# Kernel tuning notes

Hardware: AMD Instinct MI355X
Metric: run time of the kernel (lower is better)

The kernel has to match this reference:

```python
import jax, jax.numpy as jnp
import numpy as np

EMBED = 1024  # embed_dim = hidden_dim = out_dim (n_head=1)
NQ, NK = 4096, 4096
NEG = 1e16


def setup_inputs() -> dict:
    key = jax.random.key(0)
    ks = jax.random.split(key, 10)
    stdv = 1.0 / np.sqrt(EMBED)
    lin = lambda kk: jax.random.uniform(kk, (EMBED, EMBED), jnp.float32, -stdv, stdv)
    vec = lambda kk: jax.random.uniform(kk, (EMBED,), jnp.float32, -stdv, stdv)
    return {
        "q": jax.random.normal(ks[0], (NQ, EMBED), jnp.float32),
        "k": jax.random.normal(ks[1], (NK, EMBED), jnp.float32),
        "mask": jax.random.randint(ks[2], (NQ, NK), 0, 2, jnp.int32),
        "wei": jax.random.uniform(ks[3], (NQ, NK), jnp.float32),
        "Wq": lin(ks[4]), "bq": vec(ks[5]),
        "Wk": lin(ks[6]), "bk": vec(ks[7]),
        "Wp": lin(ks[8]), "bp": vec(ks[9]),
    }


def reference(q, k, mask, wei, Wq, bq, Wk, bk, Wp, bp):
    # Linear projections (torch Linear: x @ W.T + b)
    kx = k @ Wk.T + bk                      # [NK, D]
    qx = q @ Wq.T + bq                      # [NQ, D]
    # dot_product score
    score = qx @ kx.T                       # [NQ, NK]
    bias = (mask.astype(jnp.int32) - 1).astype(score.dtype) * NEG
    score = jax.nn.softmax(score + bias, axis=-1)
    # second weighted+masked softmax pass
    score = jax.nn.softmax(score * wei + bias, axis=-1)
    out = (score @ kx) @ Wp.T + bp          # [NQ, D]
    return out, score
```

## Files before the change

kernel.cpp:

```cpp
#include <hip/hip_runtime.h>


typedef __bf16 bf16;
typedef __bf16 bf16x8 __attribute__((ext_vector_type(8)));
typedef __bf16 bf16x4 __attribute__((ext_vector_type(4)));
typedef float  f32x4  __attribute__((ext_vector_type(4)));
typedef float  f32x16 __attribute__((ext_vector_type(16)));

typedef __attribute__((address_space(1))) void as1_void;
typedef __attribute__((address_space(3))) void as3_void;

#define NQ  4096
#define NKK 4096
#define EMB 1024

#define BM 128
#define BN 128
#define BK 32

__device__ __forceinline__ void gld_lds16(const void* g, void* l) {
    __builtin_amdgcn_global_load_lds((as1_void*)g, (as3_void*)l, 16, 0, 0);
}

__global__ __launch_bounds__(256) void prep_pair(
    const float* __restrict__ a, const float* __restrict__ b,
    bf16* __restrict__ ah, bf16* __restrict__ al,
    bf16* __restrict__ bh, bf16* __restrict__ bl, int n)
{
    const float* s = blockIdx.y ? b : a;
    bf16* h = blockIdx.y ? bh : ah;
    bf16* l = blockIdx.y ? bl : al;
    const int i = (blockIdx.x * 256 + threadIdx.x) * 4;
    if (i >= n) return;
    f32x4 v = *(const f32x4*)(s + i);
    bf16x4 hv, lv;
#pragma unroll
    for (int c = 0; c < 4; c++) {
        float x = v[c];
        bf16 hh = (bf16)x;
        hv[c] = hh;
        lv[c] = (bf16)(x - (float)hh);
    }
    *(bf16x4*)(h + i) = hv;
    *(bf16x4*)(l + i) = lv;
}

__global__ __launch_bounds__(256) void prep_w3(
    const float* __restrict__ w0, const float* __restrict__ w1, const float* __restrict__ w2,
    bf16* __restrict__ h0, bf16* __restrict__ l0,
    bf16* __restrict__ h1, bf16* __restrict__ l1,
    bf16* __restrict__ h2, bf16* __restrict__ l2, int n)
{
    const int z = blockIdx.y;
    const float* s = (z == 0) ? w0 : (z == 1) ? w1 : w2;
    bf16* h = (z == 0) ? h0 : (z == 1) ? h1 : h2;
    bf16* l = (z == 0) ? l0 : (z == 1) ? l1 : l2;
    const int i = (blockIdx.x * 256 + threadIdx.x) * 4;
    if (i >= n) return;
    f32x4 v = *(const f32x4*)(s + i);
    bf16x4 hv, lv;
#pragma unroll
    for (int c = 0; c < 4; c++) {
        float x = v[c];
        bf16 hh = (bf16)x;
        hv[c] = hh;
        lv[c] = (bf16)(x - (float)hh);
    }
    *(bf16x4*)(h + i) = hv;
    *(bf16x4*)(l + i) = lv;
}

__global__ __launch_bounds__(256) void transpose_bf16(
    const bf16* __restrict__ src, bf16* __restrict__ dst, int R, int C)
{
    __shared__ bf16 tile[32][33];
    const int bx = blockIdx.x * 32;
    const int by = blockIdx.y * 32;
    const int tx = threadIdx.x & 31;
    const int ty = threadIdx.x >> 5;
#pragma unroll
    for (int r = 0; r < 4; r++)
        tile[ty + 8 * r][tx] = src[(size_t)(by + ty + 8 * r) * C + bx + tx];
    __syncthreads();
#pragma unroll
    for (int r = 0; r < 4; r++)
        dst[(size_t)(bx + ty + 8 * r) * R + by + tx] = tile[tx][ty + 8 * r];
}

template<int NS, int MODE>
__global__ __launch_bounds__(256) void reduce_k(
    const float* __restrict__ P, const float* __restrict__ bias,
    float* __restrict__ of, bf16* __restrict__ oh, int n, int Nld)
{
    const int i = (blockIdx.x * 256 + threadIdx.x) * 4;
    if (i >= n) return;
    f32x4 v = *(const f32x4*)(P + i);
#pragma unroll
    for (int s = 1; s < NS; s++)
        v += *(const f32x4*)(P + (size_t)s * n + i);
    if (MODE == 1)
        v += *(const f32x4*)(bias + (i & (Nld - 1)));
    if (MODE == 0) {
        bf16x4 o;
#pragma unroll
        for (int c = 0; c < 4; c++) o[c] = (bf16)v[c];
        *(bf16x4*)(oh + i) = o;
    } else {
        *(f32x4*)(of + i) = v;
    }
}

template<int NSPLIT, int HAS_BIAS, int OUT_BF16>
__global__ __launch_bounds__(256) void gemm_bt(
    const bf16* __restrict__ A, const bf16* __restrict__ B,
    const float* __restrict__ bias,
    float* __restrict__ Cf, bf16* __restrict__ Cb,
    int M, int N, int Ksub, int lda, int ldb)
{
    __shared__ bf16 sA[BM * BK];
    __shared__ bf16 sB[BN * BK];
    const int t    = threadIdx.x;
    const int wave = t >> 6;
    const int lane = t & 63;
    const int l31  = lane & 31;
    const int lhi  = lane >> 5;
    const int wm   = wave >> 1;
    const int wn   = wave & 1;
    const int bm   = blockIdx.y * BM;
    const int bn   = blockIdx.x * BN;
    const int srow = t >> 2;
    const int gseg = (t & 3) ^ ((srow >> 1) & 3);
    const int rsw  = (l31 >> 1) & 3;
    const int kz   = (NSPLIT > 0) ? (int)blockIdx.z : 0;

    A += (size_t)kz * Ksub;
    B += (size_t)kz * Ksub;
    if (NSPLIT > 0) Cf += (size_t)kz * M * N;

    const bf16* ga = A + (size_t)(bm + srow) * lda + gseg * 8;
    const bf16* gb = B + (size_t)(bn + srow) * ldb + gseg * 8;
    char* lA = (char*)sA + wave * 1024;
    char* lB = (char*)sB + wave * 1024;

    f32x16 acc[2][2] = {};

    for (int k0 = 0; k0 < Ksub; k0 += BK) {
        __syncthreads();
        gld_lds16(ga + k0,                      lA);
        gld_lds16(ga + (size_t)64 * lda + k0,   lA + 4096);
        gld_lds16(gb + k0,                      lB);
        gld_lds16(gb + (size_t)64 * ldb + k0,   lB + 4096);
        __syncthreads();
        bf16x8 af[2][2], bfr[2][2];
#pragma unroll
        for (int mi = 0; mi < 2; mi++)
#pragma unroll
            for (int kh = 0; kh < 2; kh++)
                af[mi][kh] = *(const bf16x8*)
                    &sA[(wm * 64 + mi * 32 + l31) * BK + ((kh * 2 + lhi) ^ rsw) * 8];
#pragma unroll
        for (int nj = 0; nj < 2; nj++)
#pragma unroll
            for (int kh = 0; kh < 2; kh++)
                bfr[nj][kh] = *(const bf16x8*)
                    &sB[(wn * 64 + nj * 32 + l31) * BK + ((kh * 2 + lhi) ^ rsw) * 8];
#pragma unroll
        for (int kh = 0; kh < 2; kh++)
#pragma unroll
            for (int mi = 0; mi < 2; mi++)
#pragma unroll
                for (int nj = 0; nj < 2; nj++)
                    acc[mi][nj] = __builtin_amdgcn_mfma_f32_32x32x16_bf16(
                        af[mi][kh], bfr[nj][kh], acc[mi][nj], 0, 0, 0);
    }

#pragma unroll
    for (int mi = 0; mi < 2; mi++)
#pragma unroll
        for (int nj = 0; nj < 2; nj++) {
            const int cg = bn + wn * 64 + nj * 32 + l31;
            const float bv = HAS_BIAS ? bias[cg] : 0.0f;
#pragma unroll
            for (int r = 0; r < 16; r++) {
                const int rg = bm + wm * 64 + mi * 32 + (r & 3) + 8 * (r >> 2) + 4 * lhi;
                const float v = acc[mi][nj][r] + bv;
                const size_t idx = (size_t)rg * N + cg;
                if (NSPLIT > 0)    Cf[idx] = v;
                else if (OUT_BF16) Cb[idx] = (bf16)v;
                else               Cf[idx] = v;
            }
        }
}

template<int BATCH, int HAS_BIAS, int HILO>
__global__ __launch_bounds__(256) void gemm_bt_split(
    const bf16* __restrict__ Ah0, const bf16* __restrict__ Al0,
    const bf16* __restrict__ Bh0, const bf16* __restrict__ Bl0,
    const float* __restrict__ bias0, bf16* __restrict__ Ch0, bf16* __restrict__ Cl0,
    const bf16* __restrict__ Ah1, const bf16* __restrict__ Al1,
    const bf16* __restrict__ Bh1, const bf16* __restrict__ Bl1,
    const float* __restrict__ bias1, bf16* __restrict__ Ch1, bf16* __restrict__ Cl1,
    float* __restrict__ Cf,
    int M, int N, int K)
{
    __shared__ bf16 sAh[BM * BK], sAl[BM * BK], sBh[BN * BK], sBl[BN * BK];
    const int t    = threadIdx.x;
    const int wave = t >> 6;
    const int lane = t & 63;
    const int l31  = lane & 31;
    const int lhi  = lane >> 5;
    const int wm   = wave >> 1;
    const int wn   = wave & 1;
    const int bm   = blockIdx.y * BM;
    const int bn   = blockIdx.x * BN;
    const int srow = t >> 2;
    const int gseg = (t & 3) ^ ((srow >> 1) & 3);
    const int rsw  = (l31 >> 1) & 3;

    const int mt = BATCH ? (int)blockIdx.z : 0;

    const bf16* Ah = (BATCH && mt) ? Ah1 : Ah0;
    const bf16* Al = (BATCH && mt) ? Al1 : Al0;
    const bf16* Bh = (BATCH && mt) ? Bh1 : Bh0;
    const bf16* Bl = (BATCH && mt) ? Bl1 : Bl0;
    const float* bias = (BATCH && mt) ? bias1 : bias0;
    bf16* Ch = (BATCH && mt) ? Ch1 : Ch0;
    bf16* Cl = (BATCH && mt) ? Cl1 : Cl0;

    const size_t offA = (size_t)(bm + srow) * K + gseg * 8;
    const size_t offB = (size_t)(bn + srow) * K + gseg * 8;
    char* lAh = (char*)sAh + wave * 1024;
    char* lAl = (char*)sAl + wave * 1024;
    char* lBh = (char*)sBh + wave * 1024;
    char* lBl = (char*)sBl + wave * 1024;

    f32x16 acc[2][2] = {};

    for (int k0 = 0; k0 < K; k0 += BK) {
        __syncthreads();
        gld_lds16(Ah + offA + k0,                  lAh);
        gld_lds16(Ah + offA + (size_t)64 * K + k0, lAh + 4096);
        gld_lds16(Al + offA + k0,                  lAl);
        gld_lds16(Al + offA + (size_t)64 * K + k0, lAl + 4096);
        gld_lds16(Bh + offB + k0,                  lBh);
        gld_lds16(Bh + offB + (size_t)64 * K + k0, lBh + 4096);
        gld_lds16(Bl + offB + k0,                  lBl);
        gld_lds16(Bl + offB + (size_t)64 * K + k0, lBl + 4096);
        __syncthreads();
#pragma unroll
        for (int kh = 0; kh < 2; kh++) {
            const int ksw = ((kh * 2 + lhi) ^ rsw) * 8;
            bf16x8 ah[2], al[2], bh2[2], bl2[2];
#pragma unroll
            for (int mi = 0; mi < 2; mi++) {
                const int ro = (wm * 64 + mi * 32 + l31) * BK + ksw;
                ah[mi] = *(const bf16x8*)&sAh[ro];
                al[mi] = *(const bf16x8*)&sAl[ro];
            }
#pragma unroll
            for (int nj = 0; nj < 2; nj++) {
                const int ro = (wn * 64 + nj * 32 + l31) * BK + ksw;
                bh2[nj] = *(const bf16x8*)&sBh[ro];
                bl2[nj] = *(const bf16x8*)&sBl[ro];
            }
#pragma unroll
            for (int mi = 0; mi < 2; mi++)
#pragma unroll
                for (int nj = 0; nj < 2; nj++) {
                    acc[mi][nj] = __builtin_amdgcn_mfma_f32_32x32x16_bf16(al[mi], bh2[nj], acc[mi][nj], 0, 0, 0);
                    acc[mi][nj] = __builtin_amdgcn_mfma_f32_32x32x16_bf16(ah[mi], bl2[nj], acc[mi][nj], 0, 0, 0);
                    acc[mi][nj] = __builtin_amdgcn_mfma_f32_32x32x16_bf16(ah[mi], bh2[nj], acc[mi][nj], 0, 0, 0);
                }
        }
    }

#pragma unroll
    for (int mi = 0; mi < 2; mi++)
#pragma unroll
        for (int nj = 0; nj < 2; nj++) {
            const int cg = bn + wn * 64 + nj * 32 + l31;
            const float bv = HAS_BIAS ? bias[cg] : 0.0f;
#pragma unroll
            for (int r = 0; r < 16; r++) {
                const int rg = bm + wm * 64 + mi * 32 + (r & 3) + 8 * (r >> 2) + 4 * lhi;
                const float v = acc[mi][nj][r] + bv;
                const size_t idx = (size_t)rg * N + cg;
                if (HILO) {
                    const bf16 hh = (bf16)v;
                    Ch[idx] = hh;
                    Cl[idx] = (bf16)(v - (float)hh);
                } else {
                    Cf[idx] = v;
                }
            }
        }
}

__global__ __launch_bounds__(256, 2) void gemm_score(
    const bf16* __restrict__ Ah, const bf16* __restrict__ Al,
    const bf16* __restrict__ Bh, const bf16* __restrict__ Bl,
    float* __restrict__ Cf, int N, int K)
{
    __shared__ bf16 sAh[128 * BK], sAl[128 * BK], sBh[256 * BK], sBl[256 * BK];
    const int t    = threadIdx.x;
    const int wave = t >> 6;
    const int lane = t & 63;
    const int l31  = lane & 31;
    const int lhi  = lane >> 5;
    const int bm   = blockIdx.y * 128;
    const int bn   = blockIdx.x * 256;
    const int srow = t >> 2;
    const int gseg = (t & 3) ^ ((srow >> 1) & 3);
    const int rsw  = (l31 >> 1) & 3;

    const size_t offA = (size_t)(bm + srow) * K + gseg * 8;
    const size_t offB = (size_t)(bn + srow) * K + gseg * 8;
    char* lAh = (char*)sAh + wave * 1024;
    char* lAl = (char*)sAl + wave * 1024;
    char* lBh = (char*)sBh + wave * 1024;
    char* lBl = (char*)sBl + wave * 1024;

    f32x16 acc[4][2] = {};

    for (int k0 = 0; k0 < K; k0 += BK) {
        __syncthreads();
        gld_lds16(Ah + offA + k0,                  lAh);
        gld_lds16(Ah + offA + (size_t)64 * K + k0, lAh + 4096);
        gld_lds16(Al + offA + k0,                  lAl);
        gld_lds16(Al + offA + (size_t)64 * K + k0, lAl + 4096);
#pragma unroll
        for (int rb = 0; rb < 4; rb++) {
            gld_lds16(Bh + offB + (size_t)(64 * rb) * K + k0, lBh + rb * 4096);
            gld_lds16(Bl + offB + (size_t)(64 * rb) * K + k0, lBl + rb * 4096);
        }
        __syncthreads();
#pragma unroll
        for (int kh = 0; kh < 2; kh++) {
            const int ksw = ((kh * 2 + lhi) ^ rsw) * 8;
            bf16x8 ah[4], al[4], bh2[2], bl2[2];
#pragma unroll
            for (int mi = 0; mi < 4; mi++) {
                const int ro = (mi * 32 + l31) * BK + ksw;
                ah[mi] = *(const bf16x8*)&sAh[ro];
                al[mi] = *(const bf16x8*)&sAl[ro];
            }
#pragma unroll
            for (int nj = 0; nj < 2; nj++) {
                const int ro = (wave * 64 + nj * 32 + l31) * BK + ksw;
                bh2[nj] = *(const bf16x8*)&sBh[ro];
                bl2[nj] = *(const bf16x8*)&sBl[ro];
            }
#pragma unroll
            for (int mi = 0; mi < 4; mi++)
#pragma unroll
                for (int nj = 0; nj < 2; nj++) {
                    acc[mi][nj] = __builtin_amdgcn_mfma_f32_32x32x16_bf16(al[mi], bh2[nj], acc[mi][nj], 0, 0, 0);
                    acc[mi][nj] = __builtin_amdgcn_mfma_f32_32x32x16_bf16(ah[mi], bl2[nj], acc[mi][nj], 0, 0, 0);
                    acc[mi][nj] = __builtin_amdgcn_mfma_f32_32x32x16_bf16(ah[mi], bh2[nj], acc[mi][nj], 0, 0, 0);
                }
        }
    }

#pragma unroll
    for (int mi = 0; mi < 4; mi++)
#pragma unroll
        for (int nj = 0; nj < 2; nj++) {
            const int cg = bn + wave * 64 + nj * 32 + l31;
#pragma unroll
            for (int r = 0; r < 16; r++) {
                const int rg = bm + mi * 32 + (r & 3) + 8 * (r >> 2) + 4 * lhi;
                Cf[(size_t)rg * N + cg] = acc[mi][nj][r];
            }
        }
}

__device__ __forceinline__ float wred_max(float v) {
#pragma unroll
    for (int off = 32; off > 0; off >>= 1) v = fmaxf(v, __shfl_xor(v, off));
    return v;
}
__device__ __forceinline__ float wred_sum(float v) {
#pragma unroll
    for (int off = 32; off > 0; off >>= 1) v += __shfl_xor(v, off);
    return v;
}

__global__ __launch_bounds__(256) void softmax2_kernel(
    float* __restrict__ score, const int* __restrict__ mask,
    const float* __restrict__ wei, bf16* __restrict__ scoreb)
{
    __shared__ float sred[4];
    const int row = blockIdx.x;
    const int t   = threadIdx.x;
    const size_t base = (size_t)row * NKK;
    const int wv = t >> 6, ln = t & 63;

    float l[16], w[16];
    unsigned mb = 0;
#pragma unroll
    for (int s = 0; s < 16; s++) {
        const int j = t + (s << 8);
        l[s] = score[base + j];
        w[s] = wei[base + j];
        if (mask[base + j] != 0) mb |= 1u << s;
    }

    float mx = -__builtin_inff();
#pragma unroll
    for (int s = 0; s < 16; s++) if (mb & (1u << s)) mx = fmaxf(mx, l[s]);
    mx = wred_max(mx);
    if (ln == 0) sred[wv] = mx;
    __syncthreads();
    mx = fmaxf(fmaxf(sred[0], sred[1]), fmaxf(sred[2], sred[3]));
    __syncthreads();
    float sum = 0.f;
#pragma unroll
    for (int s = 0; s < 16; s++) {
        const float e = (mb & (1u << s)) ? __expf(l[s] - mx) : 0.f;
        l[s] = e; sum += e;
    }
    sum = wred_sum(sum);
    if (ln == 0) sred[wv] = sum;
    __syncthreads();
    sum = sred[0] + sred[1] + sred[2] + sred[3];
    __syncthreads();
    const float inv1 = 1.0f / sum;

#pragma unroll
    for (int s = 0; s < 16; s++) l[s] = l[s] * inv1 * w[s];

    float mx2 = -__builtin_inff();
#pragma unroll
    for (int s = 0; s < 16; s++) if (mb & (1u << s)) mx2 = fmaxf(mx2, l[s]);
    mx2 = wred_max(mx2);
    if (ln == 0) sred[wv] = mx2;
    __syncthreads();
    mx2 = fmaxf(fmaxf(sred[0], sred[1]), fmaxf(sred[2], sred[3]));
    __syncthreads();
    float sum2 = 0.f;
#pragma unroll
    for (int s = 0; s < 16; s++) {
        const float e = (mb & (1u << s)) ? __expf(l[s] - mx2) : 0.f;
        l[s] = e; sum2 += e;
    }
    sum2 = wred_sum(sum2);
    if (ln == 0) sred[wv] = sum2;
    __syncthreads();
    sum2 = sred[0] + sred[1] + sred[2] + sred[3];
    const float inv2 = 1.0f / sum2;

#pragma unroll
    for (int s = 0; s < 16; s++) {
        const int j = t + (s << 8);
        const float p = l[s] * inv2;
        score[base + j]  = p;
        scoreb[base + j] = (bf16)p;
    }
}

extern "C" void kernel_launch(void* const* d_in, const int* in_sizes, int n_in,
                              void* d_out, int out_size, void* d_ws, size_t ws_size,
                              hipStream_t stream)
{
    (void)in_sizes; (void)n_in; (void)out_size;
    const float* q    = (const float*)d_in[0];
    const float* k    = (const float*)d_in[1];
    const int*   mask = (const int*)  d_in[2];
    const float* wei  = (const float*)d_in[3];
    const float* Wq   = (const float*)d_in[4];
    const float* bq   = (const float*)d_in[5];
    const float* Wk   = (const float*)d_in[6];
    const float* bk   = (const float*)d_in[7];
    const float* Wp   = (const float*)d_in[8];
    const float* bp   = (const float*)d_in[9];

    float* out   = (float*)d_out;
    float* score = (float*)d_out + (size_t)NQ * EMB;

    char* ws = (char*)d_ws;
    size_t off = 0;
    auto alloc = [&](size_t bytes) -> char* {
        char* p = ws + off; off += (bytes + 255) & ~(size_t)255; return p;
    };
    const size_t n_qk = (size_t)NQ * EMB;
    const size_t n_w  = (size_t)EMB * EMB;
    const size_t n_sc = (size_t)NQ * NKK;

    bf16* qh   = (bf16*)alloc(n_qk * 2);
    bf16* ql   = (bf16*)alloc(n_qk * 2);
    bf16* kh   = (bf16*)alloc(n_qk * 2);
    bf16* kl   = (bf16*)alloc(n_qk * 2);
    bf16* qxh  = (bf16*)alloc(n_qk * 2);
    bf16* qxl  = (bf16*)alloc(n_qk * 2);
    bf16* kxh  = (bf16*)alloc(n_qk * 2);
    bf16* kxl  = (bf16*)alloc(n_qk * 2);
    bf16* Wqh  = (bf16*)alloc(n_w * 2);
    bf16* Wql  = (bf16*)alloc(n_w * 2);
    bf16* Wkh  = (bf16*)alloc(n_w * 2);
    bf16* Wkl  = (bf16*)alloc(n_w * 2);
    bf16* Wpb  = (bf16*)alloc(n_w * 2);
    bf16* Wpl  = (bf16*)alloc(n_w * 2);
    bf16* kxTb = (bf16*)alloc(n_qk * 2);
    bf16* ctxb = (bf16*)alloc(n_qk * 2);
    bf16* scoreb = (bf16*)alloc(n_sc * 2);
    const size_t base_off = off;
    float* P = (float*)alloc(2 * n_qk * 4);
    const bool ws_ok = (off <= ws_size);
    if (base_off > ws_size) return;

    const int MN = (int)n_qk;

    prep_pair<<<dim3(n_qk / 1024, 2), 256, 0, stream>>>(q, k, qh, ql, kh, kl, (int)n_qk);
    prep_w3<<<dim3(n_w / 1024, 3), 256, 0, stream>>>(
        Wq, Wk, Wp, Wqh, Wql, Wkh, Wkl, Wpb, Wpl, (int)n_w);

    gemm_bt_split<1, 1, 1><<<dim3(EMB / BN, NQ / BM, 2), 256, 0, stream>>>(
        qh, ql, Wqh, Wql, bq, qxh, qxl,
        kh, kl, Wkh, Wkl, bk, kxh, kxl,
        nullptr, NQ, EMB, EMB);

    transpose_bf16<<<dim3(EMB / 32, NKK / 32), 256, 0, stream>>>(kxh, kxTb, NKK, EMB);

    gemm_score<<<dim3(NKK / 256, NQ / 128), 256, 0, stream>>>(
        qxh, qxl, kxh, kxl, score, NKK, EMB);

    softmax2_kernel<<<dim3(NQ), 256, 0, stream>>>(score, mask, wei, scoreb);

    if (ws_ok) {
        gemm_bt<2, 0, 0><<<dim3(EMB / BN, NQ / BM, 2), 256, 0, stream>>>(
            scoreb, kxTb, nullptr, P, nullptr, NQ, EMB, NKK / 2, NKK, NKK);
        reduce_k<2, 0><<<dim3(MN / 1024), 256, 0, stream>>>(
            P, nullptr, nullptr, ctxb, MN, EMB);
    } else {
        gemm_bt<0, 0, 1><<<dim3(EMB / BN, NQ / BM), 256, 0, stream>>>(
            scoreb, kxTb, nullptr, nullptr, ctxb, NQ, EMB, NKK, NKK, NKK);
    }

    if (ws_ok) {
        gemm_bt<2, 0, 0><<<dim3(EMB / BN, NQ / BM, 2), 256, 0, stream>>>(
            ctxb, Wpb, nullptr, P, nullptr, NQ, EMB, EMB / 2, EMB, EMB);
        reduce_k<2, 1><<<dim3(MN / 1024), 256, 0, stream>>>(
            P, bp, out, nullptr, MN, EMB);
    } else {
        gemm_bt<0, 1, 0><<<dim3(EMB / BN, NQ / BM), 256, 0, stream>>>(
            ctxb, Wpb, bp, out, nullptr, NQ, EMB, EMB, EMB, EMB);
    }
}
```

Measured before the change: 503.9 us.

## Fuse mask into score GEMM epilogue, vectorize softmax, merge prep kernels

The score GEMM epilogue now reads the int mask and writes a -1e16 sentinel for masked entries, so the softmax kernel no longer loads the mask and instead rebuilds the mask bits from the sentinel. The softmax kernel switches to contiguous per-thread 16-element chunks with vector loads and stores, including packed bf16 stores. The two input-conversion kernels are merged into one launch with five grid slices. Together these cut one full pass of mask traffic and one launch, but the mask read now falls in the GEMM epilogue, and any genuine score below -1e15 would be treated as masked.

```diff
diff --git a/kernel.cpp b/kernel.cpp
--- a/kernel.cpp
+++ b/kernel.cpp
@@ -22,39 +22,25 @@
     __builtin_amdgcn_global_load_lds((as1_void*)g, (as3_void*)l, 16, 0, 0);
 }
 
-__global__ __launch_bounds__(256) void prep_pair(
-    const float* __restrict__ a, const float* __restrict__ b,
-    bf16* __restrict__ ah, bf16* __restrict__ al,
-    bf16* __restrict__ bh, bf16* __restrict__ bl, int n)
-{
-    const float* s = blockIdx.y ? b : a;
-    bf16* h = blockIdx.y ? bh : ah;
-    bf16* l = blockIdx.y ? bl : al;
-    const int i = (blockIdx.x * 256 + threadIdx.x) * 4;
-    if (i >= n) return;
-    f32x4 v = *(const f32x4*)(s + i);
-    bf16x4 hv, lv;
-#pragma unroll
-    for (int c = 0; c < 4; c++) {
-        float x = v[c];
-        bf16 hh = (bf16)x;
-        hv[c] = hh;
-        lv[c] = (bf16)(x - (float)hh);
-    }
-    *(bf16x4*)(h + i) = hv;
-    *(bf16x4*)(l + i) = lv;
-}
-
-__global__ __launch_bounds__(256) void prep_w3(
-    const float* __restrict__ w0, const float* __restrict__ w1, const float* __restrict__ w2,
-    bf16* __restrict__ h0, bf16* __restrict__ l0,
-    bf16* __restrict__ h1, bf16* __restrict__ l1,
-    bf16* __restrict__ h2, bf16* __restrict__ l2, int n)
+__global__ __launch_bounds__(256) void prep_all(
+    const float* __restrict__ q, const float* __restrict__ k,
+    const float* __restrict__ Wq, const float* __restrict__ Wk, const float* __restrict__ Wp,
+    bf16* __restrict__ qh, bf16* __restrict__ ql,
+    bf16* __restrict__ kh, bf16* __restrict__ kl,
+    bf16* __restrict__ Wqh, bf16* __restrict__ Wql,
+    bf16* __restrict__ Wkh, bf16* __restrict__ Wkl,
+    bf16* __restrict__ Wph, bf16* __restrict__ Wpl,
+    int nqk, int nw)
 {
     const int z = blockIdx.y;
-    const float* s = (z == 0) ? w0 : (z == 1) ? w1 : w2;
-    bf16* h = (z == 0) ? h0 : (z == 1) ? h1 : h2;
-    bf16* l = (z == 0) ? l0 : (z == 1) ? l1 : l2;
+    const float* s; bf16* h; bf16* l; int n;
+    switch (z) {
+        case 0:  s = q;  h = qh;  l = ql;  n = nqk; break;
+        case 1:  s = k;  h = kh;  l = kl;  n = nqk; break;
+        case 2:  s = Wq; h = Wqh; l = Wql; n = nw;  break;
+        case 3:  s = Wk; h = Wkh; l = Wkl; n = nw;  break;
+        default: s = Wp; h = Wph; l = Wpl; n = nw;  break;
+    }
     const int i = (blockIdx.x * 256 + threadIdx.x) * 4;
     if (i >= n) return;
     f32x4 v = *(const f32x4*)(s + i);
@@ -299,6 +285,7 @@
 __global__ __launch_bounds__(256, 2) void gemm_score(
     const bf16* __restrict__ Ah, const bf16* __restrict__ Al,
     const bf16* __restrict__ Bh, const bf16* __restrict__ Bl,
+    const int* __restrict__ mask,
     float* __restrict__ Cf, int N, int K)
 {
     __shared__ bf16 sAh[128 * BK], sAl[128 * BK], sBh[256 * BK], sBl[256 * BK];
@@ -369,7 +356,8 @@
 #pragma unroll
             for (int r = 0; r < 16; r++) {
                 const int rg = bm + mi * 32 + (r & 3) + 8 * (r >> 2) + 4 * lhi;
-                Cf[(size_t)rg * N + cg] = acc[mi][nj][r];
+                const size_t idx = (size_t)rg * N + cg;
+                Cf[idx] = mask[idx] ? acc[mi][nj][r] : -1e16f;
             }
         }
 }
@@ -386,24 +374,24 @@
 }
 
 __global__ __launch_bounds__(256) void softmax2_kernel(
-    float* __restrict__ score, const int* __restrict__ mask,
-    const float* __restrict__ wei, bf16* __restrict__ scoreb)
+    float* __restrict__ score, const float* __restrict__ wei,
+    bf16* __restrict__ scoreb)
 {
     __shared__ float sred[4];
     const int row = blockIdx.x;
     const int t   = threadIdx.x;
-    const size_t base = (size_t)row * NKK;
+    const size_t base = (size_t)row * NKK + (size_t)t * 16;
     const int wv = t >> 6, ln = t & 63;
 
     float l[16], w[16];
+#pragma unroll
+    for (int c = 0; c < 4; c++) {
+        *(f32x4*)(l + 4 * c) = *(const f32x4*)(score + base + 4 * c);
+        *(f32x4*)(w + 4 * c) = *(const f32x4*)(wei + base + 4 * c);
+    }
     unsigned mb = 0;
 #pragma unroll
-    for (int s = 0; s < 16; s++) {
-        const int j = t + (s << 8);
-        l[s] = score[base + j];
-        w[s] = wei[base + j];
-        if (mask[base + j] != 0) mb |= 1u << s;
-    }
+    for (int s = 0; s < 16; s++) if (l[s] > -1e15f) mb |= 1u << s;
 
     float mx = -__builtin_inff();
 #pragma unroll
@@ -450,12 +438,19 @@
     const float inv2 = 1.0f / sum2;
 
 #pragma unroll
-    for (int s = 0; s < 16; s++) {
-        const int j = t + (s << 8);
-        const float p = l[s] * inv2;
-        score[base + j]  = p;
-        scoreb[base + j] = (bf16)p;
-    }
+    for (int c = 0; c < 4; c++) {
+        f32x4 pv;
+#pragma unroll
+        for (int j = 0; j < 4; j++) pv[j] = l[4 * c + j] * inv2;
+        *(f32x4*)(score + base + 4 * c) = pv;
+#pragma unroll
+        for (int j = 0; j < 4; j++) l[4 * c + j] = pv[j];
+    }
+    bf16x8 b0, b1;
+#pragma unroll
+    for (int j = 0; j < 8; j++) { b0[j] = (bf16)l[j]; b1[j] = (bf16)l[8 + j]; }
+    *(bf16x8*)(scoreb + base)     = b0;
+    *(bf16x8*)(scoreb + base + 8) = b1;
 }
 
 extern "C" void kernel_launch(void* const* d_in, const int* in_sizes, int n_in,
@@ -510,9 +505,10 @@
 
     const int MN = (int)n_qk;
 
-    prep_pair<<<dim3(n_qk / 1024, 2), 256, 0, stream>>>(q, k, qh, ql, kh, kl, (int)n_qk);
-    prep_w3<<<dim3(n_w / 1024, 3), 256, 0, stream>>>(
-        Wq, Wk, Wp, Wqh, Wql, Wkh, Wkl, Wpb, Wpl, (int)n_w);
+    prep_all<<<dim3(n_qk / 1024, 5), 256, 0, stream>>>(
+        q, k, Wq, Wk, Wp,
+        qh, ql, kh, kl, Wqh, Wql, Wkh, Wkl, Wpb, Wpl,
+        (int)n_qk, (int)n_w);
 
     gemm_bt_split<1, 1, 1><<<dim3(EMB / BN, NQ / BM, 2), 256, 0, stream>>>(
         qh, ql, Wqh, Wql, bq, qxh, qxl,
@@ -522,9 +518,9 @@
     transpose_bf16<<<dim3(EMB / 32, NKK / 32), 256, 0, stream>>>(kxh, kxTb, NKK, EMB);
 
     gemm_score<<<dim3(NKK / 256, NQ / 128), 256, 0, stream>>>(
-        qxh, qxl, kxh, kxl, score, NKK, EMB);
-
-    softmax2_kernel<<<dim3(NQ), 256, 0, stream>>>(score, mask, wei, scoreb);
+        qxh, qxl, kxh, kxl, mask, score, NKK, EMB);
+
+    softmax2_kernel<<<dim3(NQ), 256, 0, stream>>>(score, wei, scoreb);
 
     if (ws_ok) {
         gemm_bt<2, 0, 0><<<dim3(EMB / BN, NQ / BM, 2), 256, 0, stream>>>(
```

Measured after the change: 521.3 us. 3.5% more time.
